# Optimization experiments

Hardware: AMD Instinct MI355X
Metric: run time of the kernel (lower is better)

The kernel has to match this reference:

```python
import jax, jax.numpy as jnp
import numpy as np
from jax import lax

N, IN_CH, OUT_CH, KERNEL, D = 16, 256, 256, 3, 4096
FACTOR = 2  # upsampling factor
RESAMPLE_K = (1.0, 3.0, 3.0, 1.0)


def _fir_kernel():
    # _setup_kernel: normalize to sum 1; upsample path scales by gain * factor
    k = np.asarray(RESAMPLE_K, dtype=np.float32)
    k = k / k.sum()
    return k * FACTOR  # gain = 1


def setup_inputs() -> dict:
    key = jax.random.key(0)
    k1, k2, k3 = jax.random.split(key, 3)
    x = jax.random.normal(k1, (N, IN_CH, D), dtype=jnp.float32)
    weight = jax.random.normal(k2, (OUT_CH, IN_CH, KERNEL), dtype=jnp.float32) * 0.05
    bias = jax.random.normal(k3, (OUT_CH,), dtype=jnp.float32) * 0.05
    return {"x": x, "weight": weight, "bias": bias}


def _upfirdn1d(x, k, pad0, pad1):
    # up=down=1 path of StyleGAN2 upfirdn1d: pad, then TRUE convolution with FIR k
    # (torch native impl flips k before F.conv1d). Depthwise via [N*C,1,L] reshape.
    n, c, _ = x.shape
    xp = jnp.pad(x, ((0, 0), (0, 0), (pad0, pad1)))
    kr = k[::-1][None, None, :]  # flip -> correlation == convolution
    y = lax.conv_general_dilated(
        xp.reshape(n * c, 1, -1), kr, window_strides=(1,), padding=[(0, 0)],
        dimension_numbers=("NCH", "OIH", "NCH"))
    return y.reshape(n, c, -1)


def _upsample_conv_1d(x, w):
    # torch: w reshaped/flipped/permuted then conv_transpose1d(stride=factor).
    # conv_transpose with that transformed weight == correlation with the ORIGINAL
    # w on an input dilated by `factor` with (convH-1) padding on both sides
    # (output_padding = 0 for these shapes).
    convH = w.shape[2]
    y = lax.conv_general_dilated(
        x, w, window_strides=(1,), padding=[(convH - 1, convH - 1)],
        lhs_dilation=(FACTOR,), dimension_numbers=("NCH", "OIH", "NCH"))
    k = jnp.asarray(_fir_kernel())
    p = k.shape[0] - FACTOR - (convH - 1)  # = 0 here
    pad0 = (p + 1) // 2 + FACTOR - 1
    pad1 = p // 2 + 1
    return _upfirdn1d(y, k, pad0, pad1)  # -> [N, C_out, D * FACTOR]


def reference(x, weight, bias):
    y = _upsample_conv_1d(x, weight)
    return y + bias[None, :, None]
```

## Files before the change

### kernel.cpp

```cpp
#include <hip/hip_runtime.h>
#include <hip/hip_bf16.h>

#define N_   16
#define CI_  256
#define CO_  256
#define D_   4096
#define DO_  8192
#define KTOT 768
#define XTROWS 4098
#define WT_ELEMS (512 * KTOT)
#define XT_ELEMS ((size_t)N_ * XTROWS * 256)

typedef short frag8 __attribute__((ext_vector_type(8)));
typedef float facc4 __attribute__((ext_vector_type(4)));

static __device__ __forceinline__ unsigned short f2bf(float f) {
    union { __hip_bfloat16 h; unsigned short u; } cv;
    cv.h = __float2bfloat16(f);
    return cv.u;
}

static __device__ __forceinline__ unsigned int pack2(float lo, float hi) {
    return (unsigned int)f2bf(lo) | ((unsigned int)f2bf(hi) << 16);
}

static __device__ __forceinline__ void async16(unsigned short* lds, const unsigned short* g) {
    __builtin_amdgcn_global_load_lds(
        (const __attribute__((address_space(1))) unsigned int*)g,
        (__attribute__((address_space(3))) unsigned int*)lds, 16, 0, 0);
}

#define DSR_(dst, addr, litstr) \
    asm volatile("ds_read_b128 %0, %1 offset:" litstr : "=&v"(dst) : "v"(addr))

__global__ __launch_bounds__(256) void prep_all(const float* __restrict__ x,
                                                const float* __restrict__ w,
                                                unsigned short* __restrict__ Wt,
                                                unsigned short* __restrict__ xt) {
    const int tid = threadIdx.x;

    if (blockIdx.x == 128) {
        const int ci = tid;
        #pragma unroll 2
        for (int i = 0; i < 16; ++i) {
            const int co = blockIdx.y * 16 + i;
            const float* wp = w + ((size_t)co * CI_ + ci) * 3;
            const float w0 = wp[0], w1 = wp[1], w2 = wp[2];
            const float e0 = 0.25f * w1 + 0.75f * w0;
            const float e1 = 0.75f * w2 + 0.75f * w1 + 0.25f * w0;
            const float e2 = 0.25f * w2;
            const float o0 = 0.25f * w0;
            const float o1 = 0.25f * w2 + 0.75f * w1 + 0.75f * w0;
            const float o2 = 0.75f * w2 + 0.25f * w1;
            unsigned short* pe = Wt + (size_t)(co * 2 + 0) * KTOT;
            unsigned short* po = Wt + (size_t)(co * 2 + 1) * KTOT;
            pe[0 * 256 + ci] = f2bf(e0); pe[1 * 256 + ci] = f2bf(e1); pe[2 * 256 + ci] = f2bf(e2);
            po[0 * 256 + ci] = f2bf(o0); po[1 * 256 + ci] = f2bf(o1); po[2 * 256 + ci] = f2bf(o2);
        }
        return;
    }

    __shared__ unsigned int Lp[32][133];
    const int t0  = blockIdx.x * 32;
    const int n   = blockIdx.y;
    const float* xn = x + (size_t)n * CI_ * D_;
    unsigned short* slab = xt + (size_t)n * XTROWS * 256;

    if (t0 == 0 && tid < 128)       ((unsigned int*)slab)[tid] = 0u;
    if (t0 == D_ - 32 && tid < 128) ((unsigned int*)(slab + (size_t)(XTROWS - 1) * 256))[tid] = 0u;

    const int cp_l  = tid >> 3;
    const int t_off = (tid & 7) * 4;

    #pragma unroll
    for (int p = 0; p < 4; ++p) {
        const int ci0 = p * 64 + cp_l * 2;
        float4 a = *(const float4*)(xn + (size_t)ci0 * D_ + t0 + t_off);
        float4 b = *(const float4*)(xn + (size_t)(ci0 + 1) * D_ + t0 + t_off);
        const int cp = p * 32 + cp_l;
        Lp[t_off + 0][cp] = pack2(a.x, b.x);
        Lp[t_off + 1][cp] = pack2(a.y, b.y);
        Lp[t_off + 2][cp] = pack2(a.z, b.z);
        Lp[t_off + 3][cp] = pack2(a.w, b.w);
    }
    __syncthreads();

    #pragma unroll
    for (int it = 0; it < 4; ++it) {
        const int row = it * 8 + (tid >> 5);
        const int c4  = (tid & 31) * 4;
        uint4 v;
        v.x = Lp[row][c4 + 0];
        v.y = Lp[row][c4 + 1];
        v.z = Lp[row][c4 + 2];
        v.w = Lp[row][c4 + 3];
        *(uint4*)(slab + (size_t)(1 + t0 + row) * 256 + c4 * 2) = v;
    }
}

__global__ __launch_bounds__(512, 2) void gemm_upfir8(
    const unsigned short* __restrict__ Wt, const unsigned short* __restrict__ xt,
    const float* __restrict__ bias, float* __restrict__ out)
{
    __shared__ __align__(16) unsigned short SL[65536];

    const int tid  = threadIdx.x;
    const int lane = tid & 63;
    const int wid  = tid >> 6;
    const int quad = lane >> 4;
    const int l16  = lane & 15;

    const int bt0 = blockIdx.x * 256;
    const int bm0 = blockIdx.y * 256;
    const int n   = blockIdx.z;

    const int srow = wid * 16 + (lane >> 2);
    const int cg   = (lane & 3) ^ ((lane >> 3) & 3);
    const unsigned short* sA = Wt + (size_t)(bm0 + srow) * KTOT + cg * 8;
    const unsigned short* sB = xt + (size_t)n * XTROWS * 256
                                  + (size_t)(bt0 + srow) * 256 + cg * 8;

    #define STAGE_A(u, mh) do {                                                     \
        async16(SL + (((u)&1)*16384 + (mh)*8192 + 0*4096 + wid*512),                \
                sA + (size_t)(mh)*128*KTOT + (u)*64 + 0);                           \
        async16(SL + (((u)&1)*16384 + (mh)*8192 + 1*4096 + wid*512),                \
                sA + (size_t)(mh)*128*KTOT + (u)*64 + 32); } while (0)
    #define STAGE_B(u, th) do {                                                     \
        async16(SL + (32768 + ((u)&1)*16384 + (th)*8192 + 0*4096 + wid*512),        \
                sB + (size_t)(th)*128*256 + (u)*64 + 0);                            \
        async16(SL + (32768 + ((u)&1)*16384 + (th)*8192 + 1*4096 + wid*512),        \
                sB + (size_t)(th)*128*256 + (u)*64 + 32); } while (0)

    const int swz = quad ^ ((l16 >> 1) & 3);
    const int mh  = wid & 1;
    const int wm  = mh * 128;
    const int wt  = ((wid >> 1) & 3) * 64;
    const unsigned base = (unsigned)(size_t)&SL[0];
    const unsigned aB = base + (unsigned)(mh * 16384 + l16 * 64 + swz * 16);
    const unsigned bB = base + 65536u
                      + (unsigned)(((wid >> 2) & 1) * 16384
                                   + (((wid >> 1) & 1) * 64 + l16) * 64 + swz * 16);

    facc4 acc[8][4] = {};

    STAGE_A(0, 0); STAGE_A(0, 1); STAGE_B(0, 0); STAGE_B(0, 1);
    STAGE_A(1, 0); STAGE_A(1, 1);
    asm volatile("s_waitcnt vmcnt(4)" ::: "memory");
    __builtin_amdgcn_s_barrier();

    #define MM(m, t)                                                                 \
        acc[m][t] = __builtin_amdgcn_mfma_f32_16x16x32_bf16(a[m][0], b[t][0], acc[m][t], 0, 0, 0); \
        acc[m][t] = __builtin_amdgcn_mfma_f32_16x16x32_bf16(a[m][1], b[t][1], acc[m][t], 0, 0, 0);

    #pragma unroll 2
    for (int u = 0; u < 12; ++u) {
        const unsigned au = aB + (unsigned)((u & 1) << 15);
        const unsigned bu = bB + (unsigned)((u & 1) << 15);
        frag8 a[8][2], b[4][2];

        DSR_(a[0][0], au, "0");    DSR_(a[0][1], au, "8192");
        DSR_(a[1][0], au, "1024"); DSR_(a[1][1], au, "9216");
        DSR_(a[2][0], au, "2048"); DSR_(a[2][1], au, "10240");
        DSR_(a[3][0], au, "3072"); DSR_(a[3][1], au, "11264");
        DSR_(b[0][0], bu, "0");    DSR_(b[0][1], bu, "8192");
        DSR_(b[1][0], bu, "1024"); DSR_(b[1][1], bu, "9216");
        if (u < 11) STAGE_B(u + 1, 0);
        __builtin_amdgcn_s_barrier();
        asm volatile("s_waitcnt lgkmcnt(0)" ::: "memory");
        __builtin_amdgcn_sched_barrier(0);
        __builtin_amdgcn_s_setprio(1);
        MM(0, 0) MM(1, 0) MM(2, 0) MM(3, 0)
        MM(0, 1) MM(1, 1) MM(2, 1) MM(3, 1)
        __builtin_amdgcn_s_setprio(0);
        __builtin_amdgcn_s_barrier();

        DSR_(a[4][0], au, "4096"); DSR_(a[4][1], au, "12288");
        DSR_(a[5][0], au, "5120"); DSR_(a[5][1], au, "13312");
        DSR_(a[6][0], au, "6144"); DSR_(a[6][1], au, "14336");
        DSR_(a[7][0], au, "7168"); DSR_(a[7][1], au, "15360");
        if (u < 11) STAGE_B(u + 1, 1);
        __builtin_amdgcn_s_barrier();
        asm volatile("s_waitcnt lgkmcnt(0)" ::: "memory");
        __builtin_amdgcn_sched_barrier(0);
        __builtin_amdgcn_s_setprio(1);
        MM(4, 0) MM(5, 0) MM(6, 0) MM(7, 0)
        MM(4, 1) MM(5, 1) MM(6, 1) MM(7, 1)
        __builtin_amdgcn_s_setprio(0);
        __builtin_amdgcn_s_barrier();

        DSR_(b[2][0], bu, "2048"); DSR_(b[2][1], bu, "10240");
        DSR_(b[3][0], bu, "3072"); DSR_(b[3][1], bu, "11264");
        if (u < 10) STAGE_A(u + 2, 0);
        __builtin_amdgcn_s_barrier();
        asm volatile("s_waitcnt lgkmcnt(0)" ::: "memory");
        __builtin_amdgcn_sched_barrier(0);
        __builtin_amdgcn_s_setprio(1);
        MM(4, 2) MM(5, 2) MM(6, 2) MM(7, 2)
        MM(4, 3) MM(5, 3) MM(6, 3) MM(7, 3)
        __builtin_amdgcn_s_setprio(0);
        __builtin_amdgcn_s_barrier();

        if (u < 10) STAGE_A(u + 2, 1);
        __builtin_amdgcn_s_barrier();
        __builtin_amdgcn_sched_barrier(0);
        __builtin_amdgcn_s_setprio(1);
        MM(0, 2) MM(1, 2) MM(2, 2) MM(3, 2)
        MM(0, 3) MM(1, 3) MM(2, 3) MM(3, 3)
        __builtin_amdgcn_s_setprio(0);
        if (u < 10) { asm volatile("s_waitcnt vmcnt(4)" ::: "memory"); }
        else        { asm volatile("s_waitcnt vmcnt(0)" ::: "memory"); }
        __builtin_amdgcn_s_barrier();
    }
    #undef MM
    #undef STAGE_A
    #undef STAGE_B

    #pragma unroll
    for (int m8 = 0; m8 < 8; ++m8) {
        int m0  = bm0 + wm + m8 * 16 + quad * 4;
        int co0 = m0 >> 1;
        float b0 = bias[co0];
        float b1 = bias[co0 + 1];
        #pragma unroll
        for (int t4 = 0; t4 < 4; ++t4) {
            int t = bt0 + wt + t4 * 16 + l16;
            facc4 v = acc[m8][t4];
            float* p0 = out + ((size_t)(n * CO_ + co0)) * DO_ + 2 * t;
            float* p1 = p0 + DO_;
            *(float2*)p0 = make_float2(v.x + b0, v.y + b0);
            *(float2*)p1 = make_float2(v.z + b1, v.w + b1);
        }
    }
}

__global__ __launch_bounds__(256) void upconv_fir_f32(
    const float* __restrict__ x, const float* __restrict__ w,
    const float* __restrict__ bias, float* __restrict__ out)
{
    __shared__ float ws[CI_][4];
    const int tid = threadIdx.x;
    const int co  = blockIdx.y;
    const int n   = blockIdx.z;
    {
        const float* wc = w + (size_t)co * CI_ * 3;
        ws[tid][0] = wc[tid * 3 + 0];
        ws[tid][1] = wc[tid * 3 + 1];
        ws[tid][2] = wc[tid * 3 + 2];
        ws[tid][3] = 0.f;
    }
    __syncthreads();
    const int t0 = (blockIdx.x * 256 + tid) * 8;
    const float* xn = x + (size_t)n * CI_ * D_;
    float s[10], g[9];
    #pragma unroll
    for (int k = 0; k < 10; ++k) s[k] = 0.f;
    #pragma unroll
    for (int k = 0; k < 9; ++k) g[k] = 0.f;
    #pragma unroll 2
    for (int ci = 0; ci < CI_; ++ci) {
        const float* xr = xn + ci * D_;
        float4 va = *(const float4*)(xr + t0);
        float4 vb = *(const float4*)(xr + t0 + 4);
        float  xm = (t0 > 0)      ? xr[t0 - 1] : 0.f;
        float  xp = (t0 + 8 < D_) ? xr[t0 + 8] : 0.f;
        float4 wv = *(const float4*)(&ws[ci][0]);
        const float w0 = wv.x, w1 = wv.y, w2 = wv.z;
        float xa[10];
        xa[0] = xm; xa[1] = va.x; xa[2] = va.y; xa[3] = va.z; xa[4] = va.w;
        xa[5] = vb.x; xa[6] = vb.y; xa[7] = vb.z; xa[8] = vb.w; xa[9] = xp;
        #pragma unroll
        for (int k = 0; k < 10; ++k) s[k] += w1 * xa[k];
        #pragma unroll
        for (int k = 0; k < 9; ++k)  g[k] += w0 * xa[k] + w2 * xa[k + 1];
    }
    const float b = bias[co];
    float o16[16];
    #pragma unroll
    for (int tt = 0; tt < 8; ++tt) {
        o16[2 * tt]     = 0.25f * (s[tt] + g[tt + 1]) + 0.75f * (g[tt] + s[tt + 1]) + b;
        o16[2 * tt + 1] = 0.25f * (g[tt] + s[tt + 2]) + 0.75f * (s[tt + 1] + g[tt + 1]) + b;
    }
    float* ob = out + ((size_t)n * CO_ + co) * DO_ + 2 * t0;
    *(float4*)(ob + 0)  = make_float4(o16[0],  o16[1],  o16[2],  o16[3]);
    *(float4*)(ob + 4)  = make_float4(o16[4],  o16[5],  o16[6],  o16[7]);
    *(float4*)(ob + 8)  = make_float4(o16[8],  o16[9],  o16[10], o16[11]);
    *(float4*)(ob + 12) = make_float4(o16[12], o16[13], o16[14], o16[15]);
}

extern "C" void kernel_launch(void* const* d_in, const int* in_sizes, int n_in,
                              void* d_out, int out_size, void* d_ws, size_t ws_size,
                              hipStream_t stream) {
    const float* x  = (const float*)d_in[0];
    const float* w  = (const float*)d_in[1];
    const float* b  = (const float*)d_in[2];
    float* out      = (float*)d_out;

    const size_t need = (size_t)WT_ELEMS * 2 + XT_ELEMS * 2;
    if (ws_size >= need) {
        unsigned short* Wt = (unsigned short*)d_ws;
        unsigned short* xt = Wt + WT_ELEMS;
        prep_all<<<dim3(D_ / 32 + 1, N_), 256, 0, stream>>>(x, w, Wt, xt);
        gemm_upfir8<<<dim3(D_ / 256, 2, N_), 512, 0, stream>>>(Wt, xt, b, out);
    } else {
        upconv_fir_f32<<<dim3(2, CO_, N_), 256, 0, stream>>>(x, w, b, out);
    }
}
```

Measured before the change: 234.6 us.

## Use 4-wave blocks with 128x128 per-wave tiles and fewer barriers

The GEMM block drops from 8 waves to 4, and each wave now computes a 128x128 output tile (8x8 MFMA fragments) instead of 128x64. Each thread issues twice as many async global-to-LDS copies, and the four-phase barrier schedule becomes two MFMA phases per K step with far fewer s_barriers. The aim is more register-level reuse of A and B fragments and less synchronisation overhead. In exchange the accumulators double to 256 floats per thread, and only 4 waves per CU (launch bounds 256,1) remain to hide latency, which risks register pressure or spills.

```diff
diff --git a/kernel.cpp b/kernel.cpp
--- a/kernel.cpp
+++ b/kernel.cpp
@@ -98,7 +98,7 @@
     }
 }
 
-__global__ __launch_bounds__(512, 2) void gemm_upfir8(
+__global__ __launch_bounds__(256, 1) void gemm_upfir4(
     const unsigned short* __restrict__ Wt, const unsigned short* __restrict__ xt,
     const float* __restrict__ bias, float* __restrict__ out)
 {
@@ -120,32 +120,40 @@
     const unsigned short* sB = xt + (size_t)n * XTROWS * 256
                                   + (size_t)(bt0 + srow) * 256 + cg * 8;
 
-    #define STAGE_A(u, mh) do {                                                     \
-        async16(SL + (((u)&1)*16384 + (mh)*8192 + 0*4096 + wid*512),                \
-                sA + (size_t)(mh)*128*KTOT + (u)*64 + 0);                           \
-        async16(SL + (((u)&1)*16384 + (mh)*8192 + 1*4096 + wid*512),                \
-                sA + (size_t)(mh)*128*KTOT + (u)*64 + 32); } while (0)
-    #define STAGE_B(u, th) do {                                                     \
-        async16(SL + (32768 + ((u)&1)*16384 + (th)*8192 + 0*4096 + wid*512),        \
-                sB + (size_t)(th)*128*256 + (u)*64 + 0);                            \
-        async16(SL + (32768 + ((u)&1)*16384 + (th)*8192 + 1*4096 + wid*512),        \
-                sB + (size_t)(th)*128*256 + (u)*64 + 32); } while (0)
+    #define STAGE_A(u, mh) do { const int p_ = (u) & 1;                                   \
+        async16(SL + p_*16384 + (mh)*8192 + 0*4096 + 0*2048 + wid*512,                    \
+                sA + (size_t)((mh)*128 +  0)*KTOT + (u)*64 + 0);                          \
+        async16(SL + p_*16384 + (mh)*8192 + 1*4096 + 0*2048 + wid*512,                    \
+                sA + (size_t)((mh)*128 +  0)*KTOT + (u)*64 + 32);                         \
+        async16(SL + p_*16384 + (mh)*8192 + 0*4096 + 1*2048 + wid*512,                    \
+                sA + (size_t)((mh)*128 + 64)*KTOT + (u)*64 + 0);                          \
+        async16(SL + p_*16384 + (mh)*8192 + 1*4096 + 1*2048 + wid*512,                    \
+                sA + (size_t)((mh)*128 + 64)*KTOT + (u)*64 + 32); } while (0)
+    #define STAGE_B(u, th) do { const int p_ = (u) & 1;                                   \
+        async16(SL + 32768 + p_*16384 + (th)*8192 + 0*4096 + 0*2048 + wid*512,            \
+                sB + (size_t)((th)*128 +  0)*256 + (u)*64 + 0);                           \
+        async16(SL + 32768 + p_*16384 + (th)*8192 + 1*4096 + 0*2048 + wid*512,            \
+                sB + (size_t)((th)*128 +  0)*256 + (u)*64 + 32);                          \
+        async16(SL + 32768 + p_*16384 + (th)*8192 + 0*4096 + 1*2048 + wid*512,            \
+                sB + (size_t)((th)*128 + 64)*256 + (u)*64 + 0);                           \
+        async16(SL + 32768 + p_*16384 + (th)*8192 + 1*4096 + 1*2048 + wid*512,            \
+                sB + (size_t)((th)*128 + 64)*256 + (u)*64 + 32); } while (0)
 
     const int swz = quad ^ ((l16 >> 1) & 3);
     const int mh  = wid & 1;
+    const int th  = wid >> 1;
     const int wm  = mh * 128;
-    const int wt  = ((wid >> 1) & 3) * 64;
+    const int wt  = th * 128;
     const unsigned base = (unsigned)(size_t)&SL[0];
     const unsigned aB = base + (unsigned)(mh * 16384 + l16 * 64 + swz * 16);
-    const unsigned bB = base + 65536u
-                      + (unsigned)(((wid >> 2) & 1) * 16384
-                                   + (((wid >> 1) & 1) * 64 + l16) * 64 + swz * 16);
-
-    facc4 acc[8][4] = {};
-
-    STAGE_A(0, 0); STAGE_A(0, 1); STAGE_B(0, 0); STAGE_B(0, 1);
+    const unsigned bB = base + 65536u + (unsigned)(th * 16384 + l16 * 64 + swz * 16);
+
+    facc4 acc[8][8] = {};
+
+    STAGE_A(0, 0); STAGE_A(0, 1);
+    STAGE_B(0, 0); STAGE_B(0, 1);
     STAGE_A(1, 0); STAGE_A(1, 1);
-    asm volatile("s_waitcnt vmcnt(4)" ::: "memory");
+    asm volatile("s_waitcnt vmcnt(8)" ::: "memory");
     __builtin_amdgcn_s_barrier();
 
     #define MM(m, t)                                                                 \
@@ -156,58 +164,58 @@
     for (int u = 0; u < 12; ++u) {
         const unsigned au = aB + (unsigned)((u & 1) << 15);
         const unsigned bu = bB + (unsigned)((u & 1) << 15);
-        frag8 a[8][2], b[4][2];
-
+        frag8 a[8][2], b[8][2];
+
+        DSR_(b[0][0], bu, "0");    DSR_(b[0][1], bu, "8192");
+        DSR_(b[1][0], bu, "1024"); DSR_(b[1][1], bu, "9216");
+        DSR_(b[2][0], bu, "2048"); DSR_(b[2][1], bu, "10240");
+        DSR_(b[3][0], bu, "3072"); DSR_(b[3][1], bu, "11264");
         DSR_(a[0][0], au, "0");    DSR_(a[0][1], au, "8192");
         DSR_(a[1][0], au, "1024"); DSR_(a[1][1], au, "9216");
         DSR_(a[2][0], au, "2048"); DSR_(a[2][1], au, "10240");
         DSR_(a[3][0], au, "3072"); DSR_(a[3][1], au, "11264");
-        DSR_(b[0][0], bu, "0");    DSR_(b[0][1], bu, "8192");
-        DSR_(b[1][0], bu, "1024"); DSR_(b[1][1], bu, "9216");
-        if (u < 11) STAGE_B(u + 1, 0);
-        __builtin_amdgcn_s_barrier();
+        if (u < 11) { STAGE_B(u + 1, 0); STAGE_B(u + 1, 1); }
         asm volatile("s_waitcnt lgkmcnt(0)" ::: "memory");
         __builtin_amdgcn_sched_barrier(0);
-        __builtin_amdgcn_s_setprio(1);
-        MM(0, 0) MM(1, 0) MM(2, 0) MM(3, 0)
-        MM(0, 1) MM(1, 1) MM(2, 1) MM(3, 1)
-        __builtin_amdgcn_s_setprio(0);
-        __builtin_amdgcn_s_barrier();
-
+
+        DSR_(b[4][0], bu, "4096"); DSR_(b[4][1], bu, "12288");
+        DSR_(b[5][0], bu, "5120"); DSR_(b[5][1], bu, "13312");
+        DSR_(b[6][0], bu, "6144"); DSR_(b[6][1], bu, "14336");
+        DSR_(b[7][0], bu, "7168"); DSR_(b[7][1], bu, "15360");
         DSR_(a[4][0], au, "4096"); DSR_(a[4][1], au, "12288");
         DSR_(a[5][0], au, "5120"); DSR_(a[5][1], au, "13312");
         DSR_(a[6][0], au, "6144"); DSR_(a[6][1], au, "14336");
         DSR_(a[7][0], au, "7168"); DSR_(a[7][1], au, "15360");
-        if (u < 11) STAGE_B(u + 1, 1);
-        __builtin_amdgcn_s_barrier();
+        __builtin_amdgcn_sched_barrier(0);
+
+        __builtin_amdgcn_s_setprio(1);
+        MM(0,0) MM(1,0) MM(2,0) MM(3,0)
+        MM(0,1) MM(1,1) MM(2,1) MM(3,1)
+        MM(0,2) MM(1,2) MM(2,2) MM(3,2)
+        MM(0,3) MM(1,3) MM(2,3) MM(3,3)
+        __builtin_amdgcn_s_setprio(0);
+
         asm volatile("s_waitcnt lgkmcnt(0)" ::: "memory");
         __builtin_amdgcn_sched_barrier(0);
+        __builtin_amdgcn_s_barrier();
+        if (u < 10) { STAGE_A(u + 2, 0); STAGE_A(u + 2, 1); }
+
         __builtin_amdgcn_s_setprio(1);
-        MM(4, 0) MM(5, 0) MM(6, 0) MM(7, 0)
-        MM(4, 1) MM(5, 1) MM(6, 1) MM(7, 1)
+        MM(0,4) MM(1,4) MM(2,4) MM(3,4)
+        MM(0,5) MM(1,5) MM(2,5) MM(3,5)
+        MM(0,6) MM(1,6) MM(2,6) MM(3,6)
+        MM(0,7) MM(1,7) MM(2,7) MM(3,7)
+        MM(4,4) MM(5,4) MM(6,4) MM(7,4)
+        MM(4,5) MM(5,5) MM(6,5) MM(7,5)
+        MM(4,6) MM(5,6) MM(6,6) MM(7,6)
+        MM(4,7) MM(5,7) MM(6,7) MM(7,7)
+        MM(4,0) MM(5,0) MM(6,0) MM(7,0)
+        MM(4,1) MM(5,1) MM(6,1) MM(7,1)
+        MM(4,2) MM(5,2) MM(6,2) MM(7,2)
+        MM(4,3) MM(5,3) MM(6,3) MM(7,3)
         __builtin_amdgcn_s_setprio(0);
-        __builtin_amdgcn_s_barrier();
-
-        DSR_(b[2][0], bu, "2048"); DSR_(b[2][1], bu, "10240");
-        DSR_(b[3][0], bu, "3072"); DSR_(b[3][1], bu, "11264");
-        if (u < 10) STAGE_A(u + 2, 0);
-        __builtin_amdgcn_s_barrier();
-        asm volatile("s_waitcnt lgkmcnt(0)" ::: "memory");
-        __builtin_amdgcn_sched_barrier(0);
-        __builtin_amdgcn_s_setprio(1);
-        MM(4, 2) MM(5, 2) MM(6, 2) MM(7, 2)
-        MM(4, 3) MM(5, 3) MM(6, 3) MM(7, 3)
-        __builtin_amdgcn_s_setprio(0);
-        __builtin_amdgcn_s_barrier();
-
-        if (u < 10) STAGE_A(u + 2, 1);
-        __builtin_amdgcn_s_barrier();
-        __builtin_amdgcn_sched_barrier(0);
-        __builtin_amdgcn_s_setprio(1);
-        MM(0, 2) MM(1, 2) MM(2, 2) MM(3, 2)
-        MM(0, 3) MM(1, 3) MM(2, 3) MM(3, 3)
-        __builtin_amdgcn_s_setprio(0);
-        if (u < 10) { asm volatile("s_waitcnt vmcnt(4)" ::: "memory"); }
+
+        if (u < 10) { asm volatile("s_waitcnt vmcnt(8)" ::: "memory"); }
         else        { asm volatile("s_waitcnt vmcnt(0)" ::: "memory"); }
         __builtin_amdgcn_s_barrier();
     }
@@ -222,9 +230,9 @@
         float b0 = bias[co0];
         float b1 = bias[co0 + 1];
         #pragma unroll
-        for (int t4 = 0; t4 < 4; ++t4) {
-            int t = bt0 + wt + t4 * 16 + l16;
-            facc4 v = acc[m8][t4];
+        for (int t8 = 0; t8 < 8; ++t8) {
+            int t = bt0 + wt + t8 * 16 + l16;
+            facc4 v = acc[m8][t8];
             float* p0 = out + ((size_t)(n * CO_ + co0)) * DO_ + 2 * t;
             float* p1 = p0 + DO_;
             *(float2*)p0 = make_float2(v.x + b0, v.y + b0);
@@ -300,7 +308,7 @@
         unsigned short* Wt = (unsigned short*)d_ws;
         unsigned short* xt = Wt + WT_ELEMS;
         prep_all<<<dim3(D_ / 32 + 1, N_), 256, 0, stream>>>(x, w, Wt, xt);
-        gemm_upfir8<<<dim3(D_ / 256, 2, N_), 512, 0, stream>>>(Wt, xt, b, out);
+        gemm_upfir4<<<dim3(D_ / 256, 2, N_), 256, 0, stream>>>(Wt, xt, b, out);
     } else {
         upconv_fir_f32<<<dim3(2, CO_, N_), 256, 0, stream>>>(x, w, b, out);
     }
```

After: 239.5 us. 2.1% more time.

## Restructure GEMM main loop with fine-grained lgkmcnt waits and fewer barriers

Applied to the files above, without the earlier changes.

Reorders the per-iteration LDS fragment loads so all B fragments and the first half of A are issued up front. MFMA rows then start as soon as their operands arrive, using staged s_waitcnt lgkmcnt counts instead of full drains. All global-to-LDS staging for the next tiles is moved into one block after a single barrier, which cuts the barriers per iteration from about eight to two. The intent is more overlap between LDS reads and MFMA work and less synchronisation stall. In exchange, global loads are issued later in the iteration and less interleaved with compute, and the correctness of the hand-counted lgkmcnt values depends on LDS reads completing in order.

```diff
diff --git a/kernel.cpp b/kernel.cpp
--- a/kernel.cpp
+++ b/kernel.cpp
@@ -151,6 +151,11 @@
     #define MM(m, t)                                                                 \
         acc[m][t] = __builtin_amdgcn_mfma_f32_16x16x32_bf16(a[m][0], b[t][0], acc[m][t], 0, 0, 0); \
         acc[m][t] = __builtin_amdgcn_mfma_f32_16x16x32_bf16(a[m][1], b[t][1], acc[m][t], 0, 0, 0);
+    #define MMROW(m) MM(m,0) MM(m,1) MM(m,2) MM(m,3)
+
+    #define LGKM(lit) \
+        asm volatile("s_waitcnt lgkmcnt(" lit ")" ::: "memory"); \
+        __builtin_amdgcn_sched_barrier(0);
 
     #pragma unroll 2
     for (int u = 0; u < 12; ++u) {
@@ -158,60 +163,55 @@
         const unsigned bu = bB + (unsigned)((u & 1) << 15);
         frag8 a[8][2], b[4][2];
 
+        DSR_(b[0][0], bu, "0");    DSR_(b[0][1], bu, "8192");
+        DSR_(b[1][0], bu, "1024"); DSR_(b[1][1], bu, "9216");
+        DSR_(b[2][0], bu, "2048"); DSR_(b[2][1], bu, "10240");
+        DSR_(b[3][0], bu, "3072"); DSR_(b[3][1], bu, "11264");
         DSR_(a[0][0], au, "0");    DSR_(a[0][1], au, "8192");
         DSR_(a[1][0], au, "1024"); DSR_(a[1][1], au, "9216");
         DSR_(a[2][0], au, "2048"); DSR_(a[2][1], au, "10240");
         DSR_(a[3][0], au, "3072"); DSR_(a[3][1], au, "11264");
-        DSR_(b[0][0], bu, "0");    DSR_(b[0][1], bu, "8192");
-        DSR_(b[1][0], bu, "1024"); DSR_(b[1][1], bu, "9216");
-        if (u < 11) STAGE_B(u + 1, 0);
-        __builtin_amdgcn_s_barrier();
-        asm volatile("s_waitcnt lgkmcnt(0)" ::: "memory");
-        __builtin_amdgcn_sched_barrier(0);
-        __builtin_amdgcn_s_setprio(1);
-        MM(0, 0) MM(1, 0) MM(2, 0) MM(3, 0)
-        MM(0, 1) MM(1, 1) MM(2, 1) MM(3, 1)
-        __builtin_amdgcn_s_setprio(0);
-        __builtin_amdgcn_s_barrier();
+
+        LGKM("6")
+        __builtin_amdgcn_s_setprio(1);
+        MMROW(0)
+        __builtin_amdgcn_s_setprio(0);
+        LGKM("4")
+        __builtin_amdgcn_s_setprio(1);
+        MMROW(1)
+        __builtin_amdgcn_s_setprio(0);
 
         DSR_(a[4][0], au, "4096"); DSR_(a[4][1], au, "12288");
         DSR_(a[5][0], au, "5120"); DSR_(a[5][1], au, "13312");
         DSR_(a[6][0], au, "6144"); DSR_(a[6][1], au, "14336");
         DSR_(a[7][0], au, "7168"); DSR_(a[7][1], au, "15360");
-        if (u < 11) STAGE_B(u + 1, 1);
+
+        LGKM("10")
+        __builtin_amdgcn_s_setprio(1);
+        MMROW(2)
+        __builtin_amdgcn_s_setprio(0);
+        LGKM("8")
+        __builtin_amdgcn_s_setprio(1);
+        MMROW(3)
+        __builtin_amdgcn_s_setprio(0);
+
+        LGKM("0")
         __builtin_amdgcn_s_barrier();
-        asm volatile("s_waitcnt lgkmcnt(0)" ::: "memory");
-        __builtin_amdgcn_sched_barrier(0);
-        __builtin_amdgcn_s_setprio(1);
-        MM(4, 0) MM(5, 0) MM(6, 0) MM(7, 0)
-        MM(4, 1) MM(5, 1) MM(6, 1) MM(7, 1)
-        __builtin_amdgcn_s_setprio(0);
-        __builtin_amdgcn_s_barrier();
-
-        DSR_(b[2][0], bu, "2048"); DSR_(b[2][1], bu, "10240");
-        DSR_(b[3][0], bu, "3072"); DSR_(b[3][1], bu, "11264");
-        if (u < 10) STAGE_A(u + 2, 0);
-        __builtin_amdgcn_s_barrier();
-        asm volatile("s_waitcnt lgkmcnt(0)" ::: "memory");
-        __builtin_amdgcn_sched_barrier(0);
-        __builtin_amdgcn_s_setprio(1);
-        MM(4, 2) MM(5, 2) MM(6, 2) MM(7, 2)
-        MM(4, 3) MM(5, 3) MM(6, 3) MM(7, 3)
-        __builtin_amdgcn_s_setprio(0);
-        __builtin_amdgcn_s_barrier();
-
-        if (u < 10) STAGE_A(u + 2, 1);
-        __builtin_amdgcn_s_barrier();
-        __builtin_amdgcn_sched_barrier(0);
-        __builtin_amdgcn_s_setprio(1);
-        MM(0, 2) MM(1, 2) MM(2, 2) MM(3, 2)
-        MM(0, 3) MM(1, 3) MM(2, 3) MM(3, 3)
-        __builtin_amdgcn_s_setprio(0);
+
+        if (u < 11) { STAGE_B(u + 1, 0); STAGE_B(u + 1, 1); }
+        if (u < 10) { STAGE_A(u + 2, 0); STAGE_A(u + 2, 1); }
+
+        __builtin_amdgcn_s_setprio(1);
+        MMROW(4) MMROW(5) MMROW(6) MMROW(7)
+        __builtin_amdgcn_s_setprio(0);
+
         if (u < 10) { asm volatile("s_waitcnt vmcnt(4)" ::: "memory"); }
         else        { asm volatile("s_waitcnt vmcnt(0)" ::: "memory"); }
         __builtin_amdgcn_s_barrier();
     }
     #undef MM
+    #undef MMROW
+    #undef LGKM
     #undef STAGE_A
     #undef STAGE_B
 
```

Result: no change. 234.7 us (median of 2 runs) (+0.1%).
